# Optimization experiments

Measured on AMD Instinct MI355X. Metric: run time of the kernel, lower is better.

The kernel has to match this reference:

```python
import jax, jax.numpy as jnp
import numpy as np

HIDDEN_DIM = 256
NLAT, NLON = 64, 128
BATCH, N_STATIONS = 2, 1024


def _grid_coords():
    lat = jnp.linspace(-90.0, 90.0, NLAT)
    lon = jnp.linspace(-180.0, 180.0, NLON)
    lat_mesh, lon_mesh = jnp.meshgrid(lat, lon, indexing='ij')
    return lat_mesh.reshape(-1), lon_mesh.reshape(-1)  # (n_grid,)


def setup_inputs() -> dict:
    key = jax.random.key(0)
    k1, k2, k3, k4, k5, k6 = jax.random.split(key, 6)
    station_features = jax.random.normal(k1, (BATCH, N_STATIONS, HIDDEN_DIM), dtype=jnp.float32)
    station_coords = jax.random.normal(k2, (BATCH, N_STATIONS, 3), dtype=jnp.float32)
    mask = jnp.ones((BATCH, N_STATIONS), dtype=jnp.float32)
    # distance_mlp params: Linear(3,32) -> GELU -> Linear(32,1) -> Softplus
    W1 = jax.random.normal(k3, (3, 32), dtype=jnp.float32) * (1.0 / np.sqrt(3.0))
    b1 = jax.random.normal(k4, (32,), dtype=jnp.float32) * 0.02
    W2 = jax.random.normal(k5, (32, 1), dtype=jnp.float32) * (1.0 / np.sqrt(32.0))
    b2 = jax.random.normal(k6, (1,), dtype=jnp.float32) * 0.02
    return {"station_features": station_features, "station_coords": station_coords,
            "mask": mask, "W1": W1, "b1": b1, "W2": W2, "b2": b2}


def reference(station_features, station_coords, mask, W1, b1, W2, b2):
    lat_grid, lon_grid = _grid_coords()  # (G,)
    station_lat = station_coords[:, :, 0]  # (B,S)
    station_lon = station_coords[:, :, 1]
    dlat = station_lat[:, :, None] - lat_grid[None, None, :]  # (B,S,G)
    dlon = station_lon[:, :, None] - lon_grid[None, None, :]
    dist = jnp.sqrt(dlat**2 + dlon**2 + 1e-6)
    dist_features = jnp.stack([dist, dlat, dlon], axis=-1)  # (B,S,G,3)
    h = jax.nn.gelu(dist_features @ W1 + b1, approximate=False)  # (B,S,G,32)
    weights = jax.nn.softplus((h @ W2 + b2)[..., 0])  # (B,S,G)
    weights = weights * mask[:, :, None]
    weights = jax.nn.softmax(weights, axis=1)  # over stations
    grid = jnp.einsum('bsg,bsd->bgd', weights, station_features)
    grid = grid.reshape(station_features.shape[0], NLAT, NLON, HIDDEN_DIM)
    return jnp.transpose(grid, (0, 3, 1, 2))  # (B, D, nlat, nlon)
```

## Files before the change

### kernel.cpp

```cpp
#include <hip/hip_runtime.h>
#include <math.h>

#define NLAT 64
#define NLON 128
#define HID  256
#define NSTA 1024
#define NG   (NLAT * NLON)
#define TG   16
#define SC   128
#define NCH  4
#define TABN 2048
#define TABW 4.5f

#define LOG2E 1.4426950408889634f
#define LN2   0.69314718055994531f

typedef float f32x4 __attribute__((ext_vector_type(4)));
typedef _Float16 f16x8 __attribute__((ext_vector_type(8)));

__device__ __forceinline__ float gelu_ref(float x) {
    const float p  = 0.3275911f;
    const float a1 = 0.254829592f, a2 = -0.284496736f, a3 = 1.421413741f,
                a4 = -1.453152027f, a5 = 1.061405429f;
    float z  = x * 0.70710678118654752f;
    float az = fabsf(z);
    float t  = __builtin_amdgcn_rcpf(fmaf(p, az, 1.0f));
    float poly = fmaf(fmaf(fmaf(fmaf(a5, t, a4), t, a3), t, a2), t, a1) * t;
    float e  = __builtin_amdgcn_exp2f(az * az * -LOG2E);
    float r  = fmaf(-poly, e, 1.0f);
    float erfz = copysignf(r, z);
    float hx = 0.5f * x;
    return fmaf(hx, erfz, hx);
}

__global__ __launch_bounds__(256)
void cvt_kernel(const float* __restrict__ feats,
                const float* __restrict__ W1, const float* __restrict__ b1,
                const float* __restrict__ W2, const float* __restrict__ b2p,
                _Float16* __restrict__ fhi, _Float16* __restrict__ flo,
                float* __restrict__ wbuf) {
    const int blk = blockIdx.x;
    if (blk == 256) {
        if (threadIdx.x == 0) {
            const float ISCALE = (float)TABN / TABW;
            const float CELL   = TABW / (float)TABN;
            const float gend   = gelu_ref(-((float)TABN - 0.5f) * CELL);
            float A = 0.0f, B = 0.0f, C = 0.0f, D = b2p[0];
            for (int j = 0; j < 32; ++j) {
                float a = W1[j], b = W1[32 + j], c = W1[64 + j], d = b1[j], w2 = W2[j];
                wbuf[j * 8 + 0] = a * ISCALE;
                wbuf[j * 8 + 1] = b * ISCALE;
                wbuf[j * 8 + 2] = c * ISCALE;
                wbuf[j * 8 + 3] = d * ISCALE;
                wbuf[j * 8 + 4] = w2;
                wbuf[j * 8 + 5] = 0.5f * w2 * CELL;
                wbuf[j * 8 + 6] = 0.0f;
                wbuf[j * 8 + 7] = 0.0f;
                A = fmaf(0.5f * w2, a, A);
                B = fmaf(0.5f * w2, b, B);
                C = fmaf(0.5f * w2, c, C);
                D = fmaf(0.5f * w2, d, D);
                D = fmaf(w2, gend, D);
            }
            wbuf[256] = A; wbuf[257] = B; wbuf[258] = C; wbuf[259] = D;
        }
        return;
    }
    __shared__ float tile[32][68];
    const int b  = blk >> 7;
    const int st = (blk >> 2) & 31;
    const int dt = blk & 3;
    {
        const int s  = threadIdx.x >> 3;
        const int dq = threadIdx.x & 7;
        const float* src = feats + ((size_t)(b * NSTA + st * 32 + s)) * HID + dt * 64 + dq * 8;
        float4 v0 = *(const float4*)src;
        float4 v1 = *(const float4*)(src + 4);
        *(float4*)&tile[s][dq * 8]     = v0;
        *(float4*)&tile[s][dq * 8 + 4] = v1;
    }
    __syncthreads();
    const int d  = threadIdx.x >> 2;
    const int sq = threadIdx.x & 3;
    f16x8 hi8, lo8;
#pragma unroll
    for (int k = 0; k < 8; ++k) {
        float v = tile[sq * 8 + k][d];
        _Float16 h = (_Float16)v;
        hi8[k] = h;
        lo8[k] = (_Float16)(v - (float)h);
    }
    const size_t o = ((size_t)(b * HID + dt * 64 + d)) * NSTA + st * 32 + sq * 8;
    *(f16x8*)&fhi[o] = hi8;
    *(f16x8*)&flo[o] = lo8;
}

__global__ __launch_bounds__(256, 4)
void s2g_kernel(const float* __restrict__ coords,
                const float* __restrict__ maskp,
                const float* __restrict__ wbuf,
                const _Float16* __restrict__ fhi,
                const _Float16* __restrict__ flo,
                float* __restrict__ out,
                float* __restrict__ acc1,
                float2* __restrict__ ml)
{
    __shared__ float gtab[TABN];
    __shared__ __align__(16) f16x8 fragAh[256];
    __shared__ __align__(16) f16x8 fragAl[256];
    __shared__ __align__(16) float4 wpk[32];
    __shared__ float w2t[32];
    __shared__ float w2h[32];
    __shared__ __align__(16) float wmaxW[4][TG];
    __shared__ __align__(16) float alphaS[TG];
    __shared__ __align__(16) float lred[TG][TG + 1];

    const int tid  = threadIdx.x;
    const int half = blockIdx.x >> 10;
    const int b    = (blockIdx.x >> 9) & 1;
    const int blk  = blockIdx.x & 511;
    const int lat  = blk >> 3;
    const int lon0 = (blk & 7) * TG;
    const int sbase = half * (NSTA / 2);

    const float latv = -90.0f + (180.0f / 63.0f) * (float)lat;
    const float LIM  = (float)TABN - 0.5f;
    const float CELL = TABW / (float)TABN;

    const float gend = gelu_ref(-LIM * CELL);
#pragma unroll
    for (int k = tid; k < TABN; k += 256) {
        float x = ((float)k + 0.5f) * CELL;
        gtab[k] = gelu_ref(-x) - gend;
    }
    if (tid < 32) {
        wpk[tid] = *(const float4*)&wbuf[tid * 8];
        w2t[tid] = wbuf[tid * 8 + 4];
        w2h[tid] = wbuf[tid * 8 + 5];
    }
    const f32x4 lin = *(const f32x4*)&wbuf[256];

    const int gA   = tid & (TG - 1);
    const int sgrp = tid >> 4;
    const float lonvA = -180.0f + (360.0f / 127.0f) * (float)(lon0 + gA);

    const int lane = tid & 63;
    const int wv   = tid >> 6;

    f32x4 acc[4];
#pragma unroll
    for (int t = 0; t < 4; ++t) acc[t] = (f32x4){0.0f, 0.0f, 0.0f, 0.0f};

    const float* cbase = coords + (size_t)b * NSTA * 3;
    const float* mbase = maskp  + (size_t)b * NSTA;
    const _Float16* fhb = fhi + (size_t)b * HID * NSTA;
    const _Float16* flb = flo + (size_t)b * HID * NSTA;

    float m_A = -1.0e30f;
    float l_t = 0.0f;

    __syncthreads();

    for (int c = 0; c < NCH; ++c) {
        const int s0 = sbase + c * SC;

        float dist[8], dla_[8], dlo_[8], v[8];
#pragma unroll
        for (int i = 0; i < 8; ++i) {
            const int s = s0 + sgrp * 8 + i;
            float dla = cbase[(size_t)s * 3 + 0] - latv;
            float dlo = cbase[(size_t)s * 3 + 1] - lonvA;
            dla_[i] = dla;
            dlo_[i] = dlo;
            float dss = sqrtf(fmaf(dla, dla, fmaf(dlo, dlo, 1e-6f)));
            dist[i] = dss;
            v[i] = fmaf(lin.x, dss, fmaf(lin.y, dla, fmaf(lin.z, dlo, lin.w)));
        }
#pragma unroll 2
        for (int j = 0; j < 32; ++j) {
            const float4 wq = wpk[j];
            const float  wy = w2h[j];
            float pre[8];
            float amin = 1.0e30f;
#pragma unroll
            for (int i = 0; i < 8; ++i) {
                pre[i] = fmaf(wq.x, dist[i], fmaf(wq.y, dla_[i], fmaf(wq.z, dlo_[i], wq.w)));
                v[i] = fmaf(wy, fabsf(pre[i]), v[i]);
                amin = fminf(amin, fabsf(pre[i]));
            }
            if (__any(amin < LIM)) {
                const float w2 = w2t[j];
#pragma unroll
                for (int i = 0; i < 8; ++i) {
                    float a = fminf(fabsf(pre[i]), LIM);
                    v[i] = fmaf(w2, gtab[(unsigned)a], v[i]);
                }
            }
        }
        float lmax = -3.0e38f;
#pragma unroll
        for (int i = 0; i < 8; ++i) {
            const int s = s0 + sgrp * 8 + i;
            float x  = v[i];
            float ax = fabsf(x);
            float e  = __builtin_amdgcn_exp2f(-ax * LOG2E);
            float sp = fmaxf(x, 0.0f) + __builtin_amdgcn_logf(1.0f + e) * LN2;
            v[i] = sp * mbase[s];
            lmax = fmaxf(lmax, v[i]);
        }
        float wm = lmax;
        wm = fmaxf(wm, __shfl_xor(wm, 16, 64));
        wm = fmaxf(wm, __shfl_xor(wm, 32, 64));
        if (lane < TG) wmaxW[wv][lane] = wm;
        __syncthreads();

        float cmx = fmaxf(fmaxf(wmaxW[0][gA], wmaxW[1][gA]),
                          fmaxf(wmaxW[2][gA], wmaxW[3][gA]));
        float mnew  = fmaxf(m_A, cmx);
        float alpha = __builtin_amdgcn_exp2f((m_A - mnew) * LOG2E);
        m_A = mnew;
        if (tid < TG) alphaS[tid] = alpha;

        {
            float ps = 0.0f;
            f16x8 fh, fl;
#pragma unroll
            for (int i = 0; i < 8; ++i) {
                float p = __builtin_amdgcn_exp2f((v[i] - mnew) * LOG2E);
                _Float16 h = (_Float16)p;
                fh[i] = h;
                fl[i] = (_Float16)(p - (float)h);
                ps += p;
            }
            const int idx = ((sgrp >> 2) << 6) + (((sgrp & 3) << 4) | gA);
            fragAh[idx] = fh;
            fragAl[idx] = fl;
            l_t = fmaf(l_t, alpha, ps);
        }
        __syncthreads();

        {
            const f32x4 al = *(const f32x4*)&alphaS[(lane >> 4) * 4];
#pragma unroll
            for (int t = 0; t < 4; ++t) acc[t] = acc[t] * al;

            const int srow = s0 + ((lane >> 4) * 8);
            const int dbase = wv * 64 + (lane & 15);
#pragma unroll
            for (int kc = 0; kc < 4; ++kc) {
                f16x8 ah = fragAh[(kc << 6) + lane];
                f16x8 al16 = fragAl[(kc << 6) + lane];
#pragma unroll
                for (int t = 0; t < 4; ++t) {
                    const size_t off = (size_t)(dbase + t * 16) * NSTA + srow + kc * 32;
                    f16x8 bh = *(const f16x8*)(fhb + off);
                    f16x8 bl = *(const f16x8*)(flb + off);
                    acc[t] = __builtin_amdgcn_mfma_f32_16x16x32_f16(ah, bh, acc[t], 0, 0, 0);
                    acc[t] = __builtin_amdgcn_mfma_f32_16x16x32_f16(ah, bl, acc[t], 0, 0, 0);
                    acc[t] = __builtin_amdgcn_mfma_f32_16x16x32_f16(al16, bh, acc[t], 0, 0, 0);
                }
            }
        }
    }

    lred[sgrp][gA] = l_t;
    __syncthreads();
    {
        float* dst = half ? acc1 : out;
        const int m0 = (lane >> 4) * 4;
        const size_t gbase = (size_t)lat * NLON + lon0 + m0;
#pragma unroll
        for (int t = 0; t < 4; ++t) {
            const int d = wv * 64 + t * 16 + (lane & 15);
            *reinterpret_cast<f32x4*>(dst + ((size_t)(b * HID + d)) * NG + gbase) = acc[t];
        }
        if (tid < TG) {
            float t = 0.0f;
#pragma unroll
            for (int k = 0; k < TG; ++k) t += lred[k][tid];
            ml[((half << 1) + b) * NG + lat * NLON + lon0 + tid] = make_float2(m_A, t);
        }
    }
}

__global__ __launch_bounds__(256)
void comb_kernel(float* __restrict__ out, const float* __restrict__ acc1,
                 const float2* __restrict__ ml) {
    const int x    = blockIdx.x;
    const int b    = x >> 9;
    const int lat  = (x >> 3) & 63;
    const int dseg = x & 7;
    const int lon  = threadIdx.x & 127;
    const int dsub = threadIdx.x >> 7;
    const int g    = lat * NLON + lon;

    const float2 p0 = ml[b * NG + g];
    const float2 p1 = ml[(2 + b) * NG + g];
    const float M  = fmaxf(p0.x, p1.x);
    float s0 = __builtin_amdgcn_exp2f((p0.x - M) * LOG2E);
    float s1 = __builtin_amdgcn_exp2f((p1.x - M) * LOG2E);
    const float rl = 1.0f / fmaf(p0.y, s0, p1.y * s1);
    s0 *= rl; s1 *= rl;

#pragma unroll 4
    for (int k = 0; k < 16; ++k) {
        const int d = dseg * 32 + dsub + k * 2;
        const size_t o = ((size_t)(b * HID + d)) * NG + g;
        out[o] = fmaf(out[o], s0, acc1[o] * s1);
    }
}

extern "C" void kernel_launch(void* const* d_in, const int* in_sizes, int n_in,
                              void* d_out, int out_size, void* d_ws, size_t ws_size,
                              hipStream_t stream) {
    const float* feats  = (const float*)d_in[0];
    const float* coords = (const float*)d_in[1];
    const float* maskp  = (const float*)d_in[2];
    const float* W1     = (const float*)d_in[3];
    const float* b1     = (const float*)d_in[4];
    const float* W2     = (const float*)d_in[5];
    const float* b2     = (const float*)d_in[6];
    float* out          = (float*)d_out;

    _Float16* fhi = (_Float16*)d_ws;
    _Float16* flo = fhi + (size_t)2 * HID * NSTA;
    float*  acc1 = (float*)((char*)d_ws + (size_t)2 * 1048576);
    float2* ml   = (float2*)((char*)d_ws + (size_t)2 * 1048576 + (size_t)2 * HID * NG * 4);
    float*  wbuf = (float*)((char*)d_ws + (size_t)2 * 1048576 + (size_t)2 * HID * NG * 4 + 262144);

    hipLaunchKernelGGL(cvt_kernel, dim3(257), dim3(256), 0, stream,
                       feats, W1, b1, W2, b2, fhi, flo, wbuf);
    hipLaunchKernelGGL(s2g_kernel, dim3(2048), dim3(256), 0, stream,
                       coords, maskp, wbuf, fhi, flo, out, acc1, ml);
    hipLaunchKernelGGL(comb_kernel, dim3(1024), dim3(256), 0, stream, out, acc1, ml);
}
```

Baseline: 258.4 us.

## Software-pipeline MFMA accumulation behind next chunk's weight computation using double-buffered fragments

The MFMA accumulation for chunk c-1 now runs at the start of iteration c, so matrix-core work can overlap the VALU-heavy distance-MLP and softmax math of the next chunk. The shared A-fragment buffers are double-buffered to make this safe. The per-station MLP math is rewritten on float2 vectors so the compiler can emit packed FMA instructions. The block-index mapping is also changed so latitude varies fastest across blocks. The cost is twice the fragment LDS, which may affect occupancy, and the new block order changes which blocks share cached data.

```diff
diff --git a/kernel.cpp b/kernel.cpp
--- a/kernel.cpp
+++ b/kernel.cpp
@@ -15,6 +15,7 @@
 #define LOG2E 1.4426950408889634f
 #define LN2   0.69314718055994531f
 
+typedef float f32x2 __attribute__((ext_vector_type(2)));
 typedef float f32x4 __attribute__((ext_vector_type(4)));
 typedef _Float16 f16x8 __attribute__((ext_vector_type(8)));
 
@@ -106,8 +107,8 @@
                 float2* __restrict__ ml)
 {
     __shared__ float gtab[TABN];
-    __shared__ __align__(16) f16x8 fragAh[256];
-    __shared__ __align__(16) f16x8 fragAl[256];
+    __shared__ __align__(16) f16x8 fragAh[2][256];
+    __shared__ __align__(16) f16x8 fragAl[2][256];
     __shared__ __align__(16) float4 wpk[32];
     __shared__ float w2t[32];
     __shared__ float w2h[32];
@@ -119,8 +120,8 @@
     const int half = blockIdx.x >> 10;
     const int b    = (blockIdx.x >> 9) & 1;
     const int blk  = blockIdx.x & 511;
-    const int lat  = blk >> 3;
-    const int lon0 = (blk & 7) * TG;
+    const int lat  = blk & 63;
+    const int lon0 = ((blk >> 6) & 7) * TG;
     const int sbase = half * (NSTA / 2);
 
     const float latv = -90.0f + (180.0f / 63.0f) * (float)lat;
@@ -161,52 +162,93 @@
 
     __syncthreads();
 
+#define PHASE_C(cc)                                                                \
+    {                                                                              \
+        const f32x4 alv = *(const f32x4*)&alphaS[(lane >> 4) * 4];                 \
+        _Pragma("unroll")                                                          \
+        for (int t = 0; t < 4; ++t) acc[t] = acc[t] * alv;                         \
+        const int srow = sbase + (cc) * SC + ((lane >> 4) * 8);                    \
+        const int dbase = wv * 64 + (lane & 15);                                   \
+        _Pragma("unroll")                                                          \
+        for (int kc = 0; kc < 4; ++kc) {                                           \
+            f16x8 ah   = fragAh[(cc) & 1][(kc << 6) + lane];                       \
+            f16x8 al16 = fragAl[(cc) & 1][(kc << 6) + lane];                       \
+            _Pragma("unroll")                                                      \
+            for (int t = 0; t < 4; ++t) {                                          \
+                const size_t off = (size_t)(dbase + t * 16) * NSTA + srow + kc * 32; \
+                f16x8 bh = *(const f16x8*)(fhb + off);                             \
+                f16x8 bl = *(const f16x8*)(flb + off);                             \
+                acc[t] = __builtin_amdgcn_mfma_f32_16x16x32_f16(ah, bh, acc[t], 0, 0, 0); \
+                acc[t] = __builtin_amdgcn_mfma_f32_16x16x32_f16(ah, bl, acc[t], 0, 0, 0); \
+                acc[t] = __builtin_amdgcn_mfma_f32_16x16x32_f16(al16, bh, acc[t], 0, 0, 0); \
+            }                                                                      \
+        }                                                                          \
+    }
+
     for (int c = 0; c < NCH; ++c) {
         const int s0 = sbase + c * SC;
 
-        float dist[8], dla_[8], dlo_[8], v[8];
-#pragma unroll
-        for (int i = 0; i < 8; ++i) {
-            const int s = s0 + sgrp * 8 + i;
-            float dla = cbase[(size_t)s * 3 + 0] - latv;
-            float dlo = cbase[(size_t)s * 3 + 1] - lonvA;
-            dla_[i] = dla;
-            dlo_[i] = dlo;
-            float dss = sqrtf(fmaf(dla, dla, fmaf(dlo, dlo, 1e-6f)));
-            dist[i] = dss;
-            v[i] = fmaf(lin.x, dss, fmaf(lin.y, dla, fmaf(lin.z, dlo, lin.w)));
+        if (c) PHASE_C(c - 1)
+
+        f32x2 dist2[4], dla2[4], dlo2[4], v2[4];
+#pragma unroll
+        for (int p = 0; p < 4; ++p) {
+            const int s = s0 + sgrp * 8 + p * 2;
+            float a0 = cbase[(size_t)s * 3 + 0] - latv;
+            float o0 = cbase[(size_t)s * 3 + 1] - lonvA;
+            float a1 = cbase[(size_t)s * 3 + 3] - latv;
+            float o1 = cbase[(size_t)s * 3 + 4] - lonvA;
+            dla2[p] = (f32x2){a0, a1};
+            dlo2[p] = (f32x2){o0, o1};
+            f32x2 dd = dla2[p] * dla2[p] + dlo2[p] * dlo2[p] + 1e-6f;
+            dist2[p] = (f32x2){sqrtf(dd.x), sqrtf(dd.y)};
+            v2[p] = dist2[p] * lin.x + (dla2[p] * lin.y + (dlo2[p] * lin.z + lin.w));
         }
 #pragma unroll 2
         for (int j = 0; j < 32; ++j) {
             const float4 wq = wpk[j];
             const float  wy = w2h[j];
-            float pre[8];
-            float amin = 1.0e30f;
-#pragma unroll
-            for (int i = 0; i < 8; ++i) {
-                pre[i] = fmaf(wq.x, dist[i], fmaf(wq.y, dla_[i], fmaf(wq.z, dlo_[i], wq.w)));
-                v[i] = fmaf(wy, fabsf(pre[i]), v[i]);
-                amin = fminf(amin, fabsf(pre[i]));
+            f32x2 pre[4];
+            float amin;
+            {
+                pre[0] = dist2[0] * wq.x + (dla2[0] * wq.y + (dlo2[0] * wq.z + wq.w));
+                pre[1] = dist2[1] * wq.x + (dla2[1] * wq.y + (dlo2[1] * wq.z + wq.w));
+                pre[2] = dist2[2] * wq.x + (dla2[2] * wq.y + (dlo2[2] * wq.z + wq.w));
+                pre[3] = dist2[3] * wq.x + (dla2[3] * wq.y + (dlo2[3] * wq.z + wq.w));
+                amin = fminf(fabsf(pre[0].x), fabsf(pre[0].y));
+#pragma unroll
+                for (int p = 0; p < 4; ++p) {
+                    v2[p].x = fmaf(wy, fabsf(pre[p].x), v2[p].x);
+                    v2[p].y = fmaf(wy, fabsf(pre[p].y), v2[p].y);
+                    if (p) amin = fminf(amin, fminf(fabsf(pre[p].x), fabsf(pre[p].y)));
+                }
             }
             if (__any(amin < LIM)) {
                 const float w2 = w2t[j];
 #pragma unroll
-                for (int i = 0; i < 8; ++i) {
-                    float a = fminf(fabsf(pre[i]), LIM);
-                    v[i] = fmaf(w2, gtab[(unsigned)a], v[i]);
+                for (int p = 0; p < 4; ++p) {
+                    float a0 = fminf(fabsf(pre[p].x), LIM);
+                    float a1 = fminf(fabsf(pre[p].y), LIM);
+                    v2[p].x = fmaf(w2, gtab[(unsigned)a0], v2[p].x);
+                    v2[p].y = fmaf(w2, gtab[(unsigned)a1], v2[p].y);
                 }
             }
         }
         float lmax = -3.0e38f;
-#pragma unroll
-        for (int i = 0; i < 8; ++i) {
-            const int s = s0 + sgrp * 8 + i;
-            float x  = v[i];
-            float ax = fabsf(x);
-            float e  = __builtin_amdgcn_exp2f(-ax * LOG2E);
-            float sp = fmaxf(x, 0.0f) + __builtin_amdgcn_logf(1.0f + e) * LN2;
-            v[i] = sp * mbase[s];
-            lmax = fmaxf(lmax, v[i]);
+        float v[8];
+#pragma unroll
+        for (int p = 0; p < 4; ++p) {
+            const int s = s0 + sgrp * 8 + p * 2;
+#pragma unroll
+            for (int e = 0; e < 2; ++e) {
+                float x  = e ? v2[p].y : v2[p].x;
+                float ax = fabsf(x);
+                float ee = __builtin_amdgcn_exp2f(-ax * LOG2E);
+                float sp = fmaxf(x, 0.0f) + __builtin_amdgcn_logf(1.0f + ee) * LN2;
+                float vv = sp * mbase[s + e];
+                v[p * 2 + e] = vv;
+                lmax = fmaxf(lmax, vv);
+            }
         }
         float wm = lmax;
         wm = fmaxf(wm, __shfl_xor(wm, 16, 64));
@@ -233,35 +275,15 @@
                 ps += p;
             }
             const int idx = ((sgrp >> 2) << 6) + (((sgrp & 3) << 4) | gA);
-            fragAh[idx] = fh;
-            fragAl[idx] = fl;
+            fragAh[c & 1][idx] = fh;
+            fragAl[c & 1][idx] = fl;
             l_t = fmaf(l_t, alpha, ps);
         }
         __syncthreads();
-
-        {
-            const f32x4 al = *(const f32x4*)&alphaS[(lane >> 4) * 4];
-#pragma unroll
-            for (int t = 0; t < 4; ++t) acc[t] = acc[t] * al;
-
-            const int srow = s0 + ((lane >> 4) * 8);
-            const int dbase = wv * 64 + (lane & 15);
-#pragma unroll
-            for (int kc = 0; kc < 4; ++kc) {
-                f16x8 ah = fragAh[(kc << 6) + lane];
-                f16x8 al16 = fragAl[(kc << 6) + lane];
-#pragma unroll
-                for (int t = 0; t < 4; ++t) {
-                    const size_t off = (size_t)(dbase + t * 16) * NSTA + srow + kc * 32;
-                    f16x8 bh = *(const f16x8*)(fhb + off);
-                    f16x8 bl = *(const f16x8*)(flb + off);
-                    acc[t] = __builtin_amdgcn_mfma_f32_16x16x32_f16(ah, bh, acc[t], 0, 0, 0);
-                    acc[t] = __builtin_amdgcn_mfma_f32_16x16x32_f16(ah, bl, acc[t], 0, 0, 0);
-                    acc[t] = __builtin_amdgcn_mfma_f32_16x16x32_f16(al16, bh, acc[t], 0, 0, 0);
-                }
-            }
-        }
-    }
+    }
+
+    PHASE_C(NCH - 1)
+#undef PHASE_C
 
     lred[sgrp][gA] = l_t;
     __syncthreads();
```

After: 254.3 us. No clear change (-1.6%).
